# Kernel optimization log

Hardware: AMD Instinct MI355X
Metric: run time of the kernel (lower is better)

## Reference

```python
import jax, jax.numpy as jnp
import numpy as np

D_MODEL = 1024
N_HEADS = 16
D_HEAD = D_MODEL // N_HEADS
FF = 4 * D_MODEL
B, S = 1, 2048
ROPE_BASE = 10000.0
LN_EPS = 1e-5


def setup_inputs() -> dict:
    key = jax.random.key(0)
    ks = jax.random.split(key, 12)
    sd = 0.02
    return {
        "x": jax.random.normal(ks[0], (B, S, D_MODEL), dtype=jnp.float32),
        # weights stored [in, out]
        "w_qkv": jax.random.normal(ks[1], (D_MODEL, 3 * D_MODEL), dtype=jnp.float32) * sd,
        "w_attn": jax.random.normal(ks[2], (D_MODEL, D_MODEL), dtype=jnp.float32) * sd,
        "b_attn": jnp.zeros((D_MODEL,), dtype=jnp.float32),
        "w_ff1": jax.random.normal(ks[3], (D_MODEL, FF), dtype=jnp.float32) * sd,
        "b_ff1": jnp.zeros((FF,), dtype=jnp.float32),
        "w_ff2": jax.random.normal(ks[4], (FF, D_MODEL), dtype=jnp.float32) * sd,
        "b_ff2": jnp.zeros((D_MODEL,), dtype=jnp.float32),
        "ln1_g": jnp.ones((D_MODEL,), dtype=jnp.float32),
        "ln1_b": jnp.zeros((D_MODEL,), dtype=jnp.float32),
        "ln2_g": jnp.ones((D_MODEL,), dtype=jnp.float32),
        "ln2_b": jnp.zeros((D_MODEL,), dtype=jnp.float32),
    }


def _layernorm(x, g, b):
    mu = jnp.mean(x, axis=-1, keepdims=True)
    var = jnp.mean(jnp.square(x - mu), axis=-1, keepdims=True)
    return (x - mu) * jax.lax.rsqrt(var + LN_EPS) * g + b


def _rope_cos_sin(seq_len, d_head, dtype):
    # scale=1.0 -> dynamic YaRN degenerates to vanilla RoPE with mscale=1
    inv_freq = 1.0 / (ROPE_BASE ** (jnp.arange(0, d_head, 2, dtype=jnp.float32) / d_head))
    pos = jnp.arange(seq_len, dtype=jnp.float32)
    freqs = pos[:, None] * inv_freq[None, :]          # [S, D/2]
    emb = jnp.concatenate([freqs, freqs], axis=-1)    # [S, D]
    return jnp.cos(emb).astype(dtype), jnp.sin(emb).astype(dtype)


def _rotate_half(x):
    x1, x2 = jnp.split(x, 2, axis=-1)
    return jnp.concatenate([-x2, x1], axis=-1)


def _apply_rope(q, k, cos, sin):
    # q,k: [B,S,H,D]; cos/sin: [S,D]
    c = cos[None, :, None, :]
    s = sin[None, :, None, :]
    return q * c + _rotate_half(q) * s, k * c + _rotate_half(k) * s


def _block(x, w_qkv, w_attn, b_attn, w_ff1, b_ff1, w_ff2, b_ff2,
           ln1_g, ln1_b, ln2_g, ln2_b):
    b, s, d = x.shape
    # --- attention sub-block (pre-norm) ---
    h = _layernorm(x, ln1_g, ln1_b)
    qkv = h @ w_qkv                                   # [B,S,3D]
    xq, xk, xv = jnp.split(qkv, 3, axis=-1)
    xq = xq.reshape(b, s, N_HEADS, D_HEAD)
    xk = xk.reshape(b, s, N_HEADS, D_HEAD)
    xv = xv.reshape(b, s, N_HEADS, D_HEAD)
    cos, sin = _rope_cos_sin(s, D_HEAD, x.dtype)
    xq, xk = _apply_rope(xq, xk, cos, sin)
    scale = 1.0 / np.sqrt(D_HEAD)
    scores = jnp.einsum("bqhd,bkhd->bhqk", xq, xk) * scale
    causal = jnp.tril(jnp.ones((s, s), dtype=bool))
    scores = jnp.where(causal[None, None], scores, jnp.finfo(scores.dtype).min)
    probs = jax.nn.softmax(scores, axis=-1)
    att = jnp.einsum("bhqk,bkhd->bqhd", probs, xv).reshape(b, s, d)
    x = x + (att @ w_attn + b_attn)
    # --- feed-forward sub-block (pre-norm) ---
    h2 = _layernorm(x, ln2_g, ln2_b)
    ff = jax.nn.gelu(h2 @ w_ff1 + b_ff1, approximate=False) @ w_ff2 + b_ff2
    return x + ff


def reference(x, w_qkv, w_attn, b_attn, w_ff1, b_ff1, w_ff2, b_ff2,
              ln1_g, ln1_b, ln2_g, ln2_b):
    return _block(x, w_qkv, w_attn, b_attn, w_ff1, b_ff1, w_ff2, b_ff2,
                  ln1_g, ln1_b, ln2_g, ln2_b)
```

## Files before the change

kernel.cpp:

```cpp
#include <hip/hip_runtime.h>
#include <hip/hip_bf16.h>
#include <stdint.h>

#define DM   1024
#define SEQ  2048
#define NH   16
#define DH   64
#define FFD  4096

typedef float  f32x4  __attribute__((ext_vector_type(4)));
typedef float  f32x16 __attribute__((ext_vector_type(16)));
typedef __bf16 bf16x8 __attribute__((ext_vector_type(8)));
typedef unsigned short u16;
typedef unsigned short u16x4v __attribute__((ext_vector_type(4)));
typedef unsigned short u16x8 __attribute__((ext_vector_type(8)));

__device__ __forceinline__ u16 f2bf(float f){
    unsigned int u = __builtin_bit_cast(unsigned int, f);
    u = u + 0x7FFFu + ((u >> 16) & 1u);
    return (u16)(u >> 16);
}
__device__ __forceinline__ float bf2f(u16 v){
    unsigned int u = ((unsigned int)v) << 16;
    return __builtin_bit_cast(float, u);
}
__device__ __forceinline__ f32x4 zero4(){ f32x4 v; v[0]=0.f;v[1]=0.f;v[2]=0.f;v[3]=0.f; return v; }
__device__ __forceinline__ unsigned int cvtpk(float lo, float hi){
    unsigned int r;
    asm("v_cvt_pk_bf16_f32 %0, %1, %2" : "=v"(r) : "v"(lo), "v"(hi));
    return r;
}

__device__ __forceinline__ void gload_lds16(const void* g, void* l){
    __builtin_amdgcn_global_load_lds(
        (const __attribute__((address_space(1))) unsigned int*)(uintptr_t)g,
        (__attribute__((address_space(3))) unsigned int*)(uintptr_t)l,
        16, 0, 0);
}

__global__ __launch_bounds__(256) void transall_k(const float* __restrict__ s0, u16* __restrict__ d0,
                                                  const float* __restrict__ s1, u16* __restrict__ d1,
                                                  const float* __restrict__ s2, u16* __restrict__ d2,
                                                  const float* __restrict__ s3, u16* __restrict__ d3){
    __shared__ float tile[64][65];
    const int b = blockIdx.x;
    const float* src; u16* dst; int K, N, bx, by;
    if (b < 768)      { src = s0; dst = d0; K = 1024; N = 3072; bx = b % 48;          by = b / 48; }
    else if (b < 1024){ src = s1; dst = d1; K = 1024; N = 1024; bx = (b-768) % 16;    by = (b-768) / 16; }
    else if (b < 2048){ src = s2; dst = d2; K = 1024; N = 4096; bx = (b-1024) % 64;   by = (b-1024) / 64; }
    else              { src = s3; dst = d3; K = 4096; N = 1024; bx = (b-2048) % 16;   by = (b-2048) / 16; }
    const int n0 = bx * 64, k0 = by * 64;
    const int t = threadIdx.x;
#pragma unroll
    for (int i = 0; i < 16; ++i){
        int idx = t + i * 256;
        int r = idx >> 6, c = idx & 63;
        tile[r][c] = src[(size_t)(k0 + r) * N + n0 + c];
    }
    __syncthreads();
#pragma unroll
    for (int i = 0; i < 16; ++i){
        int idx = t + i * 256;
        int r = idx >> 6, c = idx & 63;
        dst[(size_t)(n0 + r) * K + k0 + c] = f2bf(tile[c][r]);
    }
}

__global__ __launch_bounds__(256) void ln_k(const float* __restrict__ in,
                                            const float* __restrict__ gw,
                                            const float* __restrict__ bw,
                                            u16* __restrict__ out){
    const int row = blockIdx.x, t = threadIdx.x;
    f32x4 vv = *((const f32x4*)(in + (size_t)row * DM) + t);
    float v[4];
#pragma unroll
    for (int j = 0; j < 4; ++j) v[j] = vv[j];
    float s = 0.f, ss = 0.f;
#pragma unroll
    for (int j = 0; j < 4; ++j){ s += v[j]; ss += v[j] * v[j]; }
#pragma unroll
    for (int off = 1; off < 64; off <<= 1){
        s  += __shfl_xor(s,  off, 64);
        ss += __shfl_xor(ss, off, 64);
    }
    __shared__ float rs_[4], rss_[4];
    const int w = t >> 6;
    if ((t & 63) == 0){ rs_[w] = s; rss_[w] = ss; }
    __syncthreads();
    s  = rs_[0] + rs_[1] + rs_[2] + rs_[3];
    ss = rss_[0] + rss_[1] + rss_[2] + rss_[3];
    const float mean = s * (1.f / DM);
    const float var  = ss * (1.f / DM) - mean * mean;
    const float rstd = rsqrtf(var + 1e-5f);
#pragma unroll
    for (int j = 0; j < 4; ++j){
        int c = t * 4 + j;
        out[(size_t)row * DM + c] = f2bf((v[j] - mean) * rstd * gw[c] + bw[c]);
    }
}

template<int TM, int TN, int WR, int WC, int EPI>
__global__ __launch_bounds__(256) void gemm_k(const u16* __restrict__ A,
                                              const u16* __restrict__ Bt,
                                              const float* __restrict__ bias,
                                              const float* __restrict__ resid,
                                              void* __restrict__ out,
                                              u16* __restrict__ qout,
                                              u16* __restrict__ kout,
                                              u16* __restrict__ vout,
                                              int M, int N, int K){
    constexpr int MR   = TM / WR / 16;
    constexpr int NR   = TN / WC / 16;
    constexpr int AISS = (TM * 64) / 4096;
    constexpr int BISS = (TN * 64) / 4096;
    __shared__ u16 ldsAll[2 * TM * 32 + 2 * TN * 32];
    u16* ldsA = ldsAll;
    u16* ldsB = ldsAll + 2 * TM * 32;
    const int t = threadIdx.x;
    const int L = t & 63, w = t >> 6;
    const int g = L >> 4, li = L & 15;
    const int wr = w / WC, wc = w % WC;
    const int rowbase = wr * (TM / WR);
    const int colbase = wc * (TN / WC);
    const int brow = blockIdx.x * TM, bcol = blockIdx.y * TN;

    const u16* aPtr = A  + (size_t)brow * K;
    const u16* bPtr = Bt + (size_t)bcol * K;

    f32x4 acc[MR][NR];
#pragma unroll
    for (int m = 0; m < MR; ++m)
#pragma unroll
        for (int n = 0; n < NR; ++n) acc[m][n] = zero4();

    auto STAGE = [&](int buf, int ko){
#pragma unroll
        for (int i = 0; i < AISS; ++i){
            int o = i * 256 + t;
            gload_lds16(aPtr + (size_t)(o >> 2) * K + (o & 3) * 8 + ko, &ldsA[buf * TM * 32 + o * 8]);
        }
#pragma unroll
        for (int i = 0; i < BISS; ++i){
            int o = i * 256 + t;
            gload_lds16(bPtr + (size_t)(o >> 2) * K + (o & 3) * 8 + ko, &ldsB[buf * TN * 32 + o * 8]);
        }
    };

    const int KT = K >> 5;
    int cur = 0;
    STAGE(0, 0);
    __syncthreads();
    for (int kt = 0; kt < KT; ++kt){
        if (kt + 1 < KT) STAGE(cur ^ 1, (kt + 1) * 32);
        bf16x8 af[MR], bfr[NR];
#pragma unroll
        for (int m = 0; m < MR; ++m)
            af[m]  = *(const bf16x8*)&ldsA[cur * TM * 32 + (rowbase + m * 16 + li) * 32 + g * 8];
#pragma unroll
        for (int n = 0; n < NR; ++n)
            bfr[n] = *(const bf16x8*)&ldsB[cur * TN * 32 + (colbase + n * 16 + li) * 32 + g * 8];
#pragma unroll
        for (int m = 0; m < MR; ++m)
#pragma unroll
            for (int n = 0; n < NR; ++n)
                acc[m][n] = __builtin_amdgcn_mfma_f32_16x16x32_bf16(af[m], bfr[n], acc[m][n], 0, 0, 0);
        __syncthreads();
        cur ^= 1;
    }

    if constexpr (EPI == 4){
        const int colabs = bcol + colbase;
        const int part = colabs >> 10;
        if (part < 2){
            u16* dst = (part == 0) ? qout : kout;
            const int h = (colabs >> 6) & 15;
            float freq[2];
#pragma unroll
            for (int n = 0; n < 2; ++n)
                freq[n] = powf(10000.f, -(float)(n * 16 + li) * (1.f / 32.f));
#pragma unroll
            for (int m = 0; m < MR; ++m)
#pragma unroll
                for (int r = 0; r < 4; ++r){
                    const int srow = brow + rowbase + m * 16 + g * 4 + r;
                    const size_t rb = ((size_t)h * SEQ + srow) * 64;
#pragma unroll
                    for (int n = 0; n < 2; ++n){
                        const int i = n * 16 + li;
                        float lo = acc[m][n][r], hi = acc[m][n + 2][r];
                        float sn, cs;
                        sincosf((float)srow * freq[n], &sn, &cs);
                        dst[rb + i]      = f2bf(lo * cs - hi * sn);
                        dst[rb + i + 32] = f2bf(hi * cs + lo * sn);
                    }
                }
        } else {
            u16* tileT = ldsAll;
            __syncthreads();
#pragma unroll
            for (int m = 0; m < MR; ++m)
#pragma unroll
                for (int n = 0; n < NR; ++n)
#pragma unroll
                    for (int r = 0; r < 4; ++r){
                        const int row = rowbase + m * 16 + g * 4 + r;
                        const int col = colbase + n * 16 + li;
                        tileT[col * 72 + row] = f2bf(acc[m][n][r]);
                    }
            __syncthreads();
            const int dv = t >> 1, half = t & 1;
            const int habs = ((bcol + dv) >> 6) & 15;
            const int dvl = dv & 63;
            u16* vrow = vout + ((size_t)habs * 64 + dvl) * SEQ + brow + half * 32;
#pragma unroll
            for (int j = 0; j < 4; ++j)
                *(u16x8*)(vrow + j * 8) = *(const u16x8*)&tileT[dv * 72 + half * 32 + j * 8];
        }
        return;
    }

#pragma unroll
    for (int m = 0; m < MR; ++m)
#pragma unroll
        for (int n = 0; n < NR; ++n)
#pragma unroll
            for (int r = 0; r < 4; ++r){
                const int row = brow + rowbase + m * 16 + g * 4 + r;
                const int col = bcol + colbase + n * 16 + li;
                float v = acc[m][n][r];
                if constexpr (EPI == 1){
                    v += bias[col] + resid[(size_t)row * N + col];
                    ((float*)out)[(size_t)row * N + col] = v;
                } else if constexpr (EPI == 2){
                    v += bias[col];
                    v = 0.5f * v * (1.f + erff(v * 0.70710678f));
                    ((u16*)out)[(size_t)row * N + col] = f2bf(v);
                } else {
                    v += bias[col] + resid[(size_t)row * N + col];
                    ((float*)out)[(size_t)row * N + col] = v;
                }
            }
}

#define CHT 8
__global__ __launch_bounds__(256) void attn_k(const u16* __restrict__ Qh,
                                              const u16* __restrict__ Kh,
                                              const u16* __restrict__ VT,
                                              u16* __restrict__ Opart,
                                              float* __restrict__ ml){
    const int t = threadIdx.x, w = t >> 6, L = t & 63;
    const int bid = blockIdx.x;
    const int xcd = bid & 7;
    const int lj  = (bid >> 3) * 4 + w;
    const int h   = xcd * 2 + (lj & 1);
    const int jd  = lj >> 1;
    int g = 7, rem = jd;
    while (rem >= 8 * (g + 1)){ rem -= 8 * (g + 1); --g; }
    const int gp1 = g + 1;
    const int qt = 8 * g + 7 - rem / gp1;
    const int c  = rem % gp1;
    const int t0 = c * CHT;
    const int tEnd = min(t0 + CHT, qt + 1);
    const int l31 = L & 31, H = L >> 5;
    const int qbase = qt * 32;

    const u16* kB = Kh + (size_t)h * SEQ * 64;
    const u16* vB = VT + (size_t)h * 64 * SEQ;

    const u16* qrow = Qh + ((size_t)h * SEQ + qbase + l31) * 64 + H * 8;
    bf16x8 qf0 = *(const bf16x8*)(qrow);
    bf16x8 qf1 = *(const bf16x8*)(qrow + 16);
    bf16x8 qf2 = *(const bf16x8*)(qrow + 32);
    bf16x8 qf3 = *(const bf16x8*)(qrow + 48);

    const u16* krow0 = kB + (size_t)(t0 * 32 + l31) * 64 + H * 8;
    bf16x8 kc0 = *(const bf16x8*)(krow0);
    bf16x8 kc1 = *(const bf16x8*)(krow0 + 16);
    bf16x8 kc2 = *(const bf16x8*)(krow0 + 32);
    bf16x8 kc3 = *(const bf16x8*)(krow0 + 48);

    f32x16 O0, O1;
#pragma unroll
    for (int i = 0; i < 16; ++i){ O0[i] = 0.f; O1[i] = 0.f; }
    float m = -3.0e4f, lsum = 0.f;

    for (int tt = t0; tt < tEnd; ++tt){
        const u16* va0 = vB + (size_t)l31 * SEQ + tt * 32 + H * 8;
        const u16* va1 = va0 + (size_t)32 * SEQ;
        bf16x8 v00 = *(const bf16x8*)(va0);
        bf16x8 v01 = *(const bf16x8*)(va0 + 16);
        bf16x8 v10 = *(const bf16x8*)(va1);
        bf16x8 v11 = *(const bf16x8*)(va1 + 16);

        f32x16 st;
#pragma unroll
        for (int i = 0; i < 16; ++i) st[i] = 0.f;
        st = __builtin_amdgcn_mfma_f32_32x32x16_bf16(kc0, qf0, st, 0, 0, 0);
        st = __builtin_amdgcn_mfma_f32_32x32x16_bf16(kc1, qf1, st, 0, 0, 0);
        st = __builtin_amdgcn_mfma_f32_32x32x16_bf16(kc2, qf2, st, 0, 0, 0);
        st = __builtin_amdgcn_mfma_f32_32x32x16_bf16(kc3, qf3, st, 0, 0, 0);

        const bool more = (tt + 1 < tEnd);
        bf16x8 kn0, kn1, kn2, kn3;
        if (more){
            const u16* krow = kB + (size_t)((tt + 1) * 32 + l31) * 64 + H * 8;
            kn0 = *(const bf16x8*)(krow);
            kn1 = *(const bf16x8*)(krow + 16);
            kn2 = *(const bf16x8*)(krow + 32);
            kn3 = *(const bf16x8*)(krow + 48);
        }

        const bool diag = (tt == qt);
        float sv[16];
#pragma unroll
        for (int i = 0; i < 16; ++i){
            float x = st[i] * 0.125f;
            if (diag){
                int kkl = (i & 3) + 8 * (i >> 2) + 4 * H;
                if (kkl > l31) x = -3.0e4f;
            }
            sv[i] = x;
        }
        float smax = sv[0];
#pragma unroll
        for (int i = 1; i < 16; ++i) smax = fmaxf(smax, sv[i]);
        smax = fmaxf(smax, __shfl_xor(smax, 32, 64));
        const float nm = fmaxf(m, smax);
        const float alpha = __expf(m - nm);
        m = nm;
        float ps = 0.f;
#pragma unroll
        for (int i = 0; i < 16; ++i){ sv[i] = __expf(sv[i] - m); ps += sv[i]; }
        ps += __shfl_xor(ps, 32, 64);
        lsum = lsum * alpha + ps;
#pragma unroll
        for (int i = 0; i < 16; ++i){ O0[i] *= alpha; O1[i] *= alpha; }

        unsigned int A0 = cvtpk(sv[0],  sv[1]),  A1 = cvtpk(sv[2],  sv[3]);
        unsigned int B0 = cvtpk(sv[4],  sv[5]),  B1 = cvtpk(sv[6],  sv[7]);
        unsigned int C0 = cvtpk(sv[8],  sv[9]),  C1 = cvtpk(sv[10], sv[11]);
        unsigned int D0 = cvtpk(sv[12], sv[13]), D1 = cvtpk(sv[14], sv[15]);
        unsigned int eA0 = (unsigned int)__shfl_xor((int)A0, 32, 64);
        unsigned int eA1 = (unsigned int)__shfl_xor((int)A1, 32, 64);
        unsigned int eB0 = (unsigned int)__shfl_xor((int)B0, 32, 64);
        unsigned int eB1 = (unsigned int)__shfl_xor((int)B1, 32, 64);
        unsigned int eC0 = (unsigned int)__shfl_xor((int)C0, 32, 64);
        unsigned int eC1 = (unsigned int)__shfl_xor((int)C1, 32, 64);
        unsigned int eD0 = (unsigned int)__shfl_xor((int)D0, 32, 64);
        unsigned int eD1 = (unsigned int)__shfl_xor((int)D1, 32, 64);
        union Uw { unsigned int w[4]; bf16x8 v; };
        Uw f0, f1;
        f0.w[0] = H ? eB0 : A0;  f0.w[1] = H ? eB1 : A1;
        f0.w[2] = H ? B0  : eA0; f0.w[3] = H ? B1  : eA1;
        f1.w[0] = H ? eD0 : C0;  f1.w[1] = H ? eD1 : C1;
        f1.w[2] = H ? D0  : eC0; f1.w[3] = H ? D1  : eC1;

        O0 = __builtin_amdgcn_mfma_f32_32x32x16_bf16(v00, f0.v, O0, 0, 0, 0);
        O0 = __builtin_amdgcn_mfma_f32_32x32x16_bf16(v01, f1.v, O0, 0, 0, 0);
        O1 = __builtin_amdgcn_mfma_f32_32x32x16_bf16(v10, f0.v, O1, 0, 0, 0);
        O1 = __builtin_amdgcn_mfma_f32_32x32x16_bf16(v11, f1.v, O1, 0, 0, 0);

        if (more){ kc0 = kn0; kc1 = kn1; kc2 = kn2; kc3 = kn3; }
    }

    const int jobd = h * 288 + jd;
    const size_t ob = (size_t)jobd * (32 * 64);
    const int q = l31;
#pragma unroll
    for (int f = 0; f < 2; ++f){
        const int dv0 = f * 32;
#pragma unroll
        for (int k = 0; k < 4; ++k){
            u16x4v pkv;
#pragma unroll
            for (int e = 0; e < 4; ++e)
                pkv[e] = f2bf(f == 0 ? O0[k * 4 + e] : O1[k * 4 + e]);
            *(u16x4v*)(Opart + ob + (size_t)q * 64 + dv0 + 8 * k + 4 * H) = pkv;
        }
    }
    if (H == 0){
        ml[((size_t)jobd * 32 + q) * 2]     = m;
        ml[((size_t)jobd * 32 + q) * 2 + 1] = lsum;
    }
}

__global__ __launch_bounds__(256) void combine_k(const u16* __restrict__ Opart,
                                                 const float* __restrict__ ml,
                                                 u16* __restrict__ att){
    const int qt = blockIdx.x, h = blockIdx.y;
    const int g = qt >> 3, gp1 = g + 1;
    const int off = 8 * (36 - ((gp1 * (g + 2)) >> 1));
    const int jd0 = off + (8 * g + 7 - qt) * gp1;
    const int j0 = h * 288 + jd0;
    const int nact = gp1;
    const int t = threadIdx.x;
    const int q = t >> 3, dv0 = (t & 7) * 8;

    float m = -3.0e30f;
    for (int cc = 0; cc < nact; ++cc)
        m = fmaxf(m, ml[((size_t)(j0 + cc) * 32 + q) * 2]);
    float Ls = 0.f;
    float o[8];
#pragma unroll
    for (int j = 0; j < 8; ++j) o[j] = 0.f;
    for (int cc = 0; cc < nact; ++cc){
        const float mv = ml[((size_t)(j0 + cc) * 32 + q) * 2];
        const float lv = ml[((size_t)(j0 + cc) * 32 + q) * 2 + 1];
        const float wgt = __expf(mv - m);
        Ls += wgt * lv;
        const u16* src = Opart + ((size_t)(j0 + cc) * 32 + q) * 64 + dv0;
        u16x8 a = *(const u16x8*)src;
#pragma unroll
        for (int e = 0; e < 8; ++e) o[e] += wgt * bf2f(a[e]);
    }
    const float inv = 1.f / Ls;
    const int qg = qt * 32 + q;
#pragma unroll
    for (int j = 0; j < 8; ++j)
        att[(size_t)qg * DM + h * 64 + dv0 + j] = f2bf(o[j] * inv);
}

extern "C" void kernel_launch(void* const* d_in, const int* in_sizes, int n_in,
                              void* d_out, int out_size, void* d_ws, size_t ws_size,
                              hipStream_t stream){
    (void)in_sizes; (void)n_in; (void)out_size; (void)ws_size;
    const float* x      = (const float*)d_in[0];
    const float* w_qkv  = (const float*)d_in[1];
    const float* w_attn = (const float*)d_in[2];
    const float* b_attn = (const float*)d_in[3];
    const float* w_ff1  = (const float*)d_in[4];
    const float* b_ff1  = (const float*)d_in[5];
    const float* w_ff2  = (const float*)d_in[6];
    const float* b_ff2  = (const float*)d_in[7];
    const float* ln1g   = (const float*)d_in[8];
    const float* ln1b   = (const float*)d_in[9];
    const float* ln2g   = (const float*)d_in[10];
    const float* ln2b   = (const float*)d_in[11];

    char* ws = (char*)d_ws;
    const size_t MB = 1u << 20;
    u16*   T1    = (u16*)(ws + 0);
    u16*   T2    = (u16*)(ws + 6  * MB);
    u16*   T3    = (u16*)(ws + 8  * MB);
    u16*   T4    = (u16*)(ws + 16 * MB);
    u16*   h1    = (u16*)(ws + 24 * MB);
    u16*   Qh    = (u16*)(ws + 28 * MB);
    u16*   Kh    = (u16*)(ws + 32 * MB);
    u16*   VT    = (u16*)(ws + 36 * MB);
    u16*   Opart = (u16*)(ws + 40 * MB);
    float* mlbuf = (float*)(ws + 59 * MB);
    u16*   att   = (u16*)(ws + 0);
    float* x2    = (float*)(ws + 40 * MB);
    u16*   h2    = (u16*)(ws + 4  * MB);
    u16*   ff    = (u16*)(ws + 24 * MB);

    transall_k<<<3072, 256, 0, stream>>>(w_qkv, T1, w_attn, T2, w_ff1, T3, w_ff2, T4);
    ln_k<<<SEQ, 256, 0, stream>>>(x, ln1g, ln1b, h1);
    gemm_k<64,128,2,2,4><<<dim3(32, 24), 256, 0, stream>>>(h1, T1, nullptr, nullptr, nullptr,
                                                           Qh, Kh, VT, SEQ, 3072, 1024);
    attn_k<<<1152, 256, 0, stream>>>(Qh, Kh, VT, Opart, mlbuf);
    combine_k<<<dim3(64, 16), 256, 0, stream>>>(Opart, mlbuf, att);
    gemm_k<64,64,2,2,1><<<dim3(32, 16), 256, 0, stream>>>(att, T2, b_attn, x, x2,
                                                          nullptr, nullptr, nullptr, SEQ, 1024, 1024);
    ln_k<<<SEQ, 256, 0, stream>>>(x2, ln2g, ln2b, h2);
    gemm_k<64,128,1,4,2><<<dim3(32, 32), 256, 0, stream>>>(h2, T3, b_ff1, nullptr, ff,
                                                           nullptr, nullptr, nullptr, SEQ, 4096, 1024);
    gemm_k<64,64,2,2,3><<<dim3(32, 16), 256, 0, stream>>>(ff, T4, b_ff2, x2, (float*)d_out,
                                                          nullptr, nullptr, nullptr, SEQ, 1024, 4096);
}
```

Measured before the change: 195.0 us.

## Halve attention key chunk size, switch softmax to exp2, tree reductions

Splits each attention query tile's keys into chunks of 4 tiles instead of 8. This roughly doubles the number of split-KV jobs, giving more parallelism and shorter per-wave serial loops, at the cost of more partial outputs for the combine kernel to merge. Softmax now uses exp2 with log2e folded into the scale, max and sum use tree reductions, and a launch bounds occupancy hint is added. The K prefetch of the next tile is removed, and workspace offsets are rearranged to fit the larger partial buffer.

```diff
diff --git a/kernel.cpp b/kernel.cpp
--- a/kernel.cpp
+++ b/kernel.cpp
@@ -242,22 +242,24 @@
             }
 }
 
-#define CHT 8
-__global__ __launch_bounds__(256) void attn_k(const u16* __restrict__ Qh,
-                                              const u16* __restrict__ Kh,
-                                              const u16* __restrict__ VT,
-                                              u16* __restrict__ Opart,
-                                              float* __restrict__ ml){
+#define CHT 4
+#define JPH 544
+#define SCL2 0.18033688011112042f
+__global__ __launch_bounds__(256, 6) void attn_k(const u16* __restrict__ Qh,
+                                                 const u16* __restrict__ Kh,
+                                                 const u16* __restrict__ VT,
+                                                 u16* __restrict__ Opart,
+                                                 float* __restrict__ ml){
     const int t = threadIdx.x, w = t >> 6, L = t & 63;
     const int bid = blockIdx.x;
     const int xcd = bid & 7;
     const int lj  = (bid >> 3) * 4 + w;
     const int h   = xcd * 2 + (lj & 1);
     const int jd  = lj >> 1;
-    int g = 7, rem = jd;
-    while (rem >= 8 * (g + 1)){ rem -= 8 * (g + 1); --g; }
+    int g = 15, rem = jd;
+    while (rem >= 4 * (g + 1)){ rem -= 4 * (g + 1); --g; }
     const int gp1 = g + 1;
-    const int qt = 8 * g + 7 - rem / gp1;
+    const int qt = 4 * g + 3 - rem / gp1;
     const int c  = rem % gp1;
     const int t0 = c * CHT;
     const int tEnd = min(t0 + CHT, qt + 1);
@@ -273,18 +275,17 @@
     bf16x8 qf2 = *(const bf16x8*)(qrow + 32);
     bf16x8 qf3 = *(const bf16x8*)(qrow + 48);
 
-    const u16* krow0 = kB + (size_t)(t0 * 32 + l31) * 64 + H * 8;
-    bf16x8 kc0 = *(const bf16x8*)(krow0);
-    bf16x8 kc1 = *(const bf16x8*)(krow0 + 16);
-    bf16x8 kc2 = *(const bf16x8*)(krow0 + 32);
-    bf16x8 kc3 = *(const bf16x8*)(krow0 + 48);
-
     f32x16 O0, O1;
 #pragma unroll
     for (int i = 0; i < 16; ++i){ O0[i] = 0.f; O1[i] = 0.f; }
     float m = -3.0e4f, lsum = 0.f;
 
     for (int tt = t0; tt < tEnd; ++tt){
+        const u16* krow = kB + (size_t)(tt * 32 + l31) * 64 + H * 8;
+        bf16x8 kc0 = *(const bf16x8*)(krow);
+        bf16x8 kc1 = *(const bf16x8*)(krow + 16);
+        bf16x8 kc2 = *(const bf16x8*)(krow + 32);
+        bf16x8 kc3 = *(const bf16x8*)(krow + 48);
         const u16* va0 = vB + (size_t)l31 * SEQ + tt * 32 + H * 8;
         const u16* va1 = va0 + (size_t)32 * SEQ;
         bf16x8 v00 = *(const bf16x8*)(va0);
@@ -300,37 +301,35 @@
         st = __builtin_amdgcn_mfma_f32_32x32x16_bf16(kc2, qf2, st, 0, 0, 0);
         st = __builtin_amdgcn_mfma_f32_32x32x16_bf16(kc3, qf3, st, 0, 0, 0);
 
-        const bool more = (tt + 1 < tEnd);
-        bf16x8 kn0, kn1, kn2, kn3;
-        if (more){
-            const u16* krow = kB + (size_t)((tt + 1) * 32 + l31) * 64 + H * 8;
-            kn0 = *(const bf16x8*)(krow);
-            kn1 = *(const bf16x8*)(krow + 16);
-            kn2 = *(const bf16x8*)(krow + 32);
-            kn3 = *(const bf16x8*)(krow + 48);
-        }
-
         const bool diag = (tt == qt);
         float sv[16];
 #pragma unroll
         for (int i = 0; i < 16; ++i){
-            float x = st[i] * 0.125f;
+            float x = st[i] * SCL2;
             if (diag){
                 int kkl = (i & 3) + 8 * (i >> 2) + 4 * H;
                 if (kkl > l31) x = -3.0e4f;
             }
             sv[i] = x;
         }
-        float smax = sv[0];
-#pragma unroll
-        for (int i = 1; i < 16; ++i) smax = fmaxf(smax, sv[i]);
+        float mx[8];
+#pragma unroll
+        for (int i = 0; i < 8; ++i) mx[i] = fmaxf(sv[i], sv[i + 8]);
+#pragma unroll
+        for (int i = 0; i < 4; ++i) mx[i] = fmaxf(mx[i], mx[i + 4]);
+        float smax = fmaxf(fmaxf(mx[0], mx[1]), fmaxf(mx[2], mx[3]));
         smax = fmaxf(smax, __shfl_xor(smax, 32, 64));
         const float nm = fmaxf(m, smax);
-        const float alpha = __expf(m - nm);
+        const float alpha = exp2f(m - nm);
         m = nm;
-        float ps = 0.f;
-#pragma unroll
-        for (int i = 0; i < 16; ++i){ sv[i] = __expf(sv[i] - m); ps += sv[i]; }
+#pragma unroll
+        for (int i = 0; i < 16; ++i) sv[i] = exp2f(sv[i] - m);
+        float sm8[8];
+#pragma unroll
+        for (int i = 0; i < 8; ++i) sm8[i] = sv[i] + sv[i + 8];
+#pragma unroll
+        for (int i = 0; i < 4; ++i) sm8[i] += sm8[i + 4];
+        float ps = (sm8[0] + sm8[1]) + (sm8[2] + sm8[3]);
         ps += __shfl_xor(ps, 32, 64);
         lsum = lsum * alpha + ps;
 #pragma unroll
@@ -359,11 +358,9 @@
         O0 = __builtin_amdgcn_mfma_f32_32x32x16_bf16(v01, f1.v, O0, 0, 0, 0);
         O1 = __builtin_amdgcn_mfma_f32_32x32x16_bf16(v10, f0.v, O1, 0, 0, 0);
         O1 = __builtin_amdgcn_mfma_f32_32x32x16_bf16(v11, f1.v, O1, 0, 0, 0);
-
-        if (more){ kc0 = kn0; kc1 = kn1; kc2 = kn2; kc3 = kn3; }
-    }
-
-    const int jobd = h * 288 + jd;
+    }
+
+    const int jobd = h * JPH + jd;
     const size_t ob = (size_t)jobd * (32 * 64);
     const int q = l31;
 #pragma unroll
@@ -388,10 +385,10 @@
                                                  const float* __restrict__ ml,
                                                  u16* __restrict__ att){
     const int qt = blockIdx.x, h = blockIdx.y;
-    const int g = qt >> 3, gp1 = g + 1;
-    const int off = 8 * (36 - ((gp1 * (g + 2)) >> 1));
-    const int jd0 = off + (8 * g + 7 - qt) * gp1;
-    const int j0 = h * 288 + jd0;
+    const int g = qt >> 2, gp1 = g + 1;
+    const int off = 4 * (136 - ((gp1 * (g + 2)) >> 1));
+    const int jd0 = off + (4 * g + 3 - qt) * gp1;
+    const int j0 = h * JPH + jd0;
     const int nact = gp1;
     const int t = threadIdx.x;
     const int q = t >> 3, dv0 = (t & 7) * 8;
@@ -406,7 +403,7 @@
     for (int cc = 0; cc < nact; ++cc){
         const float mv = ml[((size_t)(j0 + cc) * 32 + q) * 2];
         const float lv = ml[((size_t)(j0 + cc) * 32 + q) * 2 + 1];
-        const float wgt = __expf(mv - m);
+        const float wgt = exp2f(mv - m);
         Ls += wgt * lv;
         const u16* src = Opart + ((size_t)(j0 + cc) * 32 + q) * 64 + dv0;
         u16x8 a = *(const u16x8*)src;
@@ -448,17 +445,17 @@
     u16*   Kh    = (u16*)(ws + 32 * MB);
     u16*   VT    = (u16*)(ws + 36 * MB);
     u16*   Opart = (u16*)(ws + 40 * MB);
-    float* mlbuf = (float*)(ws + 59 * MB);
+    float* mlbuf = (float*)(ws + 76 * MB);
     u16*   att   = (u16*)(ws + 0);
-    float* x2    = (float*)(ws + 40 * MB);
+    float* x2    = (float*)(ws + 24 * MB);
     u16*   h2    = (u16*)(ws + 4  * MB);
-    u16*   ff    = (u16*)(ws + 24 * MB);
+    u16*   ff    = (u16*)(ws + 40 * MB);
 
     transall_k<<<3072, 256, 0, stream>>>(w_qkv, T1, w_attn, T2, w_ff1, T3, w_ff2, T4);
     ln_k<<<SEQ, 256, 0, stream>>>(x, ln1g, ln1b, h1);
     gemm_k<64,128,2,2,4><<<dim3(32, 24), 256, 0, stream>>>(h1, T1, nullptr, nullptr, nullptr,
                                                            Qh, Kh, VT, SEQ, 3072, 1024);
-    attn_k<<<1152, 256, 0, stream>>>(Qh, Kh, VT, Opart, mlbuf);
+    attn_k<<<2176, 256, 0, stream>>>(Qh, Kh, VT, Opart, mlbuf);
     combine_k<<<dim3(64, 16), 256, 0, stream>>>(Opart, mlbuf, att);
     gemm_k<64,64,2,2,1><<<dim3(32, 16), 256, 0, stream>>>(att, T2, b_attn, x, x2,
                                                           nullptr, nullptr, nullptr, SEQ, 1024, 1024);
```

After: 225.2 us. 15.5% more time.
